# Kernel tuning notes

Hardware: AMD Instinct MI355X
Metric: run time of the kernel (lower is better)

Reference implementation:

```python
import jax, jax.numpy as jnp
import numpy as np

N = 50000      # nodes
E = 800000     # edges (before self-loops)
NFEATS = 256
NHIDS = 32
NHEADS = 8
NOUT = 128
NEG_SLOPE = 0.2


def leaky_relu(x, slope=NEG_SLOPE):
    return jnp.where(x >= 0, x, slope * x)


def gat_layer(x, src, dst, W, a_src, a_dst, b, heads, out_ch, concat):
    """PyG GATConv: h = xW; e_ij = LeakyReLU(a_s.h_j + a_d.h_i); softmax over
    edges grouped by destination; out_i = sum_j alpha_ij h_j (+bias)."""
    n = x.shape[0]
    h = (x @ W.T).reshape(n, heads, out_ch)            # [N,H,C]
    al_s = jnp.einsum('nhc,hc->nh', h, a_src)          # [N,H]
    al_d = jnp.einsum('nhc,hc->nh', h, a_dst)          # [N,H]
    e = leaky_relu(al_s[src] + al_d[dst])              # [E',H]
    e_max = jax.ops.segment_max(e, dst, num_segments=n)
    e_max = jnp.where(jnp.isfinite(e_max), e_max, 0.0)
    ex = jnp.exp(e - e_max[dst])
    denom = jax.ops.segment_sum(ex, dst, num_segments=n)
    alpha = ex / (denom[dst] + 1e-16)                  # [E',H]
    msg = h[src] * alpha[:, :, None]                   # [E',H,C]
    out = jax.ops.segment_sum(msg, dst, num_segments=n)  # [N,H,C]
    if concat:
        out = out.reshape(n, heads * out_ch)
    else:
        out = out.mean(axis=1)
    return out + b


def setup_inputs() -> dict:
    key = jax.random.key(0)
    ks = jax.random.split(key, 12)
    edge_index = jax.random.randint(ks[0], (2, E), 0, N, dtype=jnp.int64)
    x = jax.random.normal(ks[1], (N, NFEATS), dtype=jnp.float32)
    s1 = 1.0 / np.sqrt(NFEATS)
    W1 = jax.random.uniform(ks[2], (NHEADS * NHIDS, NFEATS), jnp.float32, -s1, s1)
    att_src1 = jax.random.normal(ks[3], (NHEADS, NHIDS), jnp.float32) * 0.1
    att_dst1 = jax.random.normal(ks[4], (NHEADS, NHIDS), jnp.float32) * 0.1
    b1 = jnp.zeros((NHEADS * NHIDS,), jnp.float32)
    s2 = 1.0 / np.sqrt(NHEADS * NHIDS)
    W2 = jax.random.uniform(ks[5], (NOUT, NHEADS * NHIDS), jnp.float32, -s2, s2)
    att_src2 = jax.random.normal(ks[6], (1, NOUT), jnp.float32) * 0.1
    att_dst2 = jax.random.normal(ks[7], (1, NOUT), jnp.float32) * 0.1
    b2 = jnp.zeros((NOUT,), jnp.float32)
    return {"edge_index": edge_index, "x": x,
            "W1": W1, "att_src1": att_src1, "att_dst1": att_dst1, "b1": b1,
            "W2": W2, "att_src2": att_src2, "att_dst2": att_dst2, "b2": b2}


def reference(edge_index, x, W1, att_src1, att_dst1, b1, W2, att_src2, att_dst2, b2):
    n = x.shape[0]
    loops = jnp.arange(n, dtype=edge_index.dtype)
    src = jnp.concatenate([edge_index[0], loops])  # PyG adds self-loops
    dst = jnp.concatenate([edge_index[1], loops])
    h = gat_layer(x, src, dst, W1, att_src1, att_dst1, b1, NHEADS, NHIDS, True)
    h = leaky_relu(h)  # module activation, slope 0.2
    # dropout(p=0.6, train=False) -> identity in eval mode
    out = gat_layer(h, src, dst, W2, att_src2, att_dst2, b2, 1, NOUT, True)
    return out
```

## Files before the change

kernel.cpp:

```cpp
#include <hip/hip_runtime.h>
#include <hip/hip_bf16.h>
#include <math.h>

#define NN 50000
#define EE 800000
#define ET 850000
#define NFEATS 256
#define NHIDS 32
#define NHEADS 8
#define NOUT 128

typedef __attribute__((ext_vector_type(8))) short bf16x8;
typedef __attribute__((ext_vector_type(4))) float f32x4;
typedef __attribute__((ext_vector_type(8))) unsigned short ushort8_t;

__device__ inline ushort f2bf(float x) {
    __hip_bfloat16 b = __float2bfloat16(x);
    return *reinterpret_cast<ushort*>(&b);
}
__device__ inline float bf2f(ushort u) {
    unsigned v = ((unsigned)u) << 16;
    return __builtin_bit_cast(float, v);
}
__device__ inline float bflo(unsigned u) {
    return __builtin_bit_cast(float, u << 16);
}
__device__ inline float bfhi(unsigned u) {
    return __builtin_bit_cast(float, u & 0xffff0000u);
}

#define NW1 (256 * 256)
#define NW2 (128 * 256)
__global__ void k_prep(const int* __restrict__ ei, int* __restrict__ deg,
                       const float* __restrict__ W1, ushort* __restrict__ W1h,
                       ushort* __restrict__ W1l,
                       const float* __restrict__ W2, ushort* __restrict__ W2h,
                       ushort* __restrict__ W2l) {
    int i = blockIdx.x * blockDim.x + threadIdx.x;
    if (i < ET) {
        int d = (i < EE) ? ei[EE + i] : (i - EE);
        atomicAdd(&deg[d], 1);
    } else if (i < ET + NW1) {
        int j = i - ET;
        float v = W1[j];
        ushort h = f2bf(v);
        W1h[j] = h;
        W1l[j] = f2bf(v - bf2f(h));
    } else if (i < ET + NW1 + NW2) {
        int j = i - ET - NW1;
        float v = W2[j];
        ushort h = f2bf(v);
        W2h[j] = h;
        W2l[j] = f2bf(v - bf2f(h));
    }
}

__global__ void k_scan_block(const int* __restrict__ deg, int* __restrict__ offsets,
                             int* __restrict__ bsum, int n) {
    __shared__ int lds[1024];
    int i = blockIdx.x * 1024 + threadIdx.x;
    int v = (i < n) ? deg[i] : 0;
    lds[threadIdx.x] = v;
    __syncthreads();
    for (int off = 1; off < 1024; off <<= 1) {
        int t = 0;
        if ((int)threadIdx.x >= off) t = lds[threadIdx.x - off];
        __syncthreads();
        lds[threadIdx.x] += t;
        __syncthreads();
    }
    if (i < n) offsets[i] = lds[threadIdx.x] - v;
    if (threadIdx.x == 1023) bsum[blockIdx.x] = lds[1023];
}

__global__ void k_scan_bsums(int* __restrict__ bsum, int nb) {
    int t = threadIdx.x;
    int v0 = (t < nb) ? bsum[t] : 0;
    int v = v0;
    for (int off = 1; off < 64; off <<= 1) {
        int u = __shfl_up(v, off, 64);
        if (t >= off) v += u;
    }
    if (t < nb) bsum[t] = v - v0;
}

__global__ void k_add_off(int* __restrict__ offsets, const int* __restrict__ bsum,
                          int n, int total) {
    int i = blockIdx.x * blockDim.x + threadIdx.x;
    if (i < n) offsets[i] += bsum[i >> 10];
    if (i == 0) offsets[n] = total;
}

__global__ void k_scatter(const int* __restrict__ ei, const int* __restrict__ offsets,
                          int* __restrict__ cursor, int* __restrict__ srcs) {
    int e = blockIdx.x * blockDim.x + threadIdx.x;
    if (e >= ET) return;
    int d, s;
    if (e < EE) { d = ei[EE + e]; s = ei[e]; }
    else        { d = e - EE;     s = e - EE; }
    int pos = offsets[d] + atomicAdd(&cursor[d], 1);
    srcs[pos] = s;
}

template <int TBN>
__global__ __launch_bounds__(512) void gemm_fused(const float* __restrict__ A,
                                                  const ushort* __restrict__ Wh,
                                                  const ushort* __restrict__ Wl,
                                                  ushort* __restrict__ Cb,
                                                  float* __restrict__ als,
                                                  float* __restrict__ ald,
                                                  const float* __restrict__ aS,
                                                  const float* __restrict__ aD,
                                                  int M) {
    constexpr int K = 256;
    constexpr int WN = TBN / 4;
    constexpr int NF = WN / 16;
    __shared__ ushort Ah[128][40], Al[128][40];
    __shared__ ushort Bh[TBN][40], Bl[TBN][40];
    __shared__ float att_red[256];

    int tid = threadIdx.x;
    int wid = tid >> 6, lane = tid & 63;
    int wm = wid >> 2, wn = wid & 3;
    int m0 = blockIdx.x * 128;

    f32x4 acc[4][NF];
#pragma unroll
    for (int i = 0; i < 4; i++)
#pragma unroll
        for (int j = 0; j < NF; j++) acc[i][j] = (f32x4){0.f, 0.f, 0.f, 0.f};

    for (int k0 = 0; k0 < K; k0 += 32) {
#pragma unroll
        for (int i = 0; i < 2; i++) {
            int s = tid + 512 * i;
            int r = s >> 3, c4 = s & 7;
            float4 v = make_float4(0.f, 0.f, 0.f, 0.f);
            if (m0 + r < M) v = *(const float4*)(A + (size_t)(m0 + r) * K + k0 + c4 * 4);
            ushort4 hi, lo;
            hi.x = f2bf(v.x); lo.x = f2bf(v.x - bf2f(hi.x));
            hi.y = f2bf(v.y); lo.y = f2bf(v.y - bf2f(hi.y));
            hi.z = f2bf(v.z); lo.z = f2bf(v.z - bf2f(hi.z));
            hi.w = f2bf(v.w); lo.w = f2bf(v.w - bf2f(hi.w));
            *(ushort4*)&Ah[r][c4 * 4] = hi;
            *(ushort4*)&Al[r][c4 * 4] = lo;
        }
        if constexpr (TBN == 256) {
            int r = tid >> 1, c16 = (tid & 1) * 16;
            const ushort* gh = Wh + (size_t)r * K + k0 + c16;
            const ushort* gl = Wl + (size_t)r * K + k0 + c16;
            *(ushort8_t*)&Bh[r][c16]     = *(const ushort8_t*)gh;
            *(ushort8_t*)&Bh[r][c16 + 8] = *(const ushort8_t*)(gh + 8);
            *(ushort8_t*)&Bl[r][c16]     = *(const ushort8_t*)gl;
            *(ushort8_t*)&Bl[r][c16 + 8] = *(const ushort8_t*)(gl + 8);
        } else {
            int s = tid & 255;
            int r = s >> 1, c16 = (s & 1) * 16;
            const ushort* gp = ((tid < 256) ? Wh : Wl) + (size_t)r * K + k0 + c16;
            ushort* lp = ((tid < 256) ? &Bh[r][c16] : &Bl[r][c16]);
            *(ushort8_t*)lp       = *(const ushort8_t*)gp;
            *(ushort8_t*)(lp + 8) = *(const ushort8_t*)(gp + 8);
        }
        __syncthreads();

        int koff = (lane >> 4) * 8;
        int rsel = lane & 15;
        bf16x8 ah[4], al[4], bh[NF], bl[NF];
#pragma unroll
        for (int mf = 0; mf < 4; mf++) {
            int r = wm * 64 + mf * 16 + rsel;
            ah[mf] = *(const bf16x8*)&Ah[r][koff];
            al[mf] = *(const bf16x8*)&Al[r][koff];
        }
#pragma unroll
        for (int nf = 0; nf < NF; nf++) {
            int c = wn * WN + nf * 16 + rsel;
            bh[nf] = *(const bf16x8*)&Bh[c][koff];
            bl[nf] = *(const bf16x8*)&Bl[c][koff];
        }
#pragma unroll
        for (int mf = 0; mf < 4; mf++)
#pragma unroll
            for (int nf = 0; nf < NF; nf++) {
                acc[mf][nf] = __builtin_amdgcn_mfma_f32_16x16x32_bf16(ah[mf], bh[nf], acc[mf][nf], 0, 0, 0);
                acc[mf][nf] = __builtin_amdgcn_mfma_f32_16x16x32_bf16(ah[mf], bl[nf], acc[mf][nf], 0, 0, 0);
                acc[mf][nf] = __builtin_amdgcn_mfma_f32_16x16x32_bf16(al[mf], bh[nf], acc[mf][nf], 0, 0, 0);
            }
        __syncthreads();
    }

    int l15 = lane & 15, lhi = lane >> 4;

#pragma unroll
    for (int mf = 0; mf < 4; mf++) {
        int gr0 = m0 + wm * 64 + mf * 16 + lhi * 4;
#pragma unroll
        for (int nf = 0; nf < NF; nf++) {
            int gc = wn * WN + nf * 16 + l15;
#pragma unroll
            for (int j = 0; j < 4; j++)
                if (gr0 + j < M) Cb[(size_t)(gr0 + j) * TBN + gc] = f2bf(acc[mf][nf][j]);
        }
    }

    if constexpr (TBN == 256) {
        float as0 = aS[wn * 64 + l15],      as0b = aS[wn * 64 + 16 + l15];
        float as1 = aS[wn * 64 + 32 + l15], as1b = aS[wn * 64 + 48 + l15];
        float ad0 = aD[wn * 64 + l15],      ad0b = aD[wn * 64 + 16 + l15];
        float ad1 = aD[wn * 64 + 32 + l15], ad1b = aD[wn * 64 + 48 + l15];
#pragma unroll
        for (int mf = 0; mf < 4; mf++) {
#pragma unroll
            for (int j = 0; j < 4; j++) {
                float ps0 = acc[mf][0][j] * as0 + acc[mf][1][j] * as0b;
                float ps1 = acc[mf][2][j] * as1 + acc[mf][3][j] * as1b;
                float pd0 = acc[mf][0][j] * ad0 + acc[mf][1][j] * ad0b;
                float pd1 = acc[mf][2][j] * ad1 + acc[mf][3][j] * ad1b;
#pragma unroll
                for (int off = 1; off <= 8; off <<= 1) {
                    ps0 += __shfl_xor(ps0, off, 64);
                    ps1 += __shfl_xor(ps1, off, 64);
                    pd0 += __shfl_xor(pd0, off, 64);
                    pd1 += __shfl_xor(pd1, off, 64);
                }
                int gr = m0 + wm * 64 + mf * 16 + lhi * 4 + j;
                if (l15 == 0 && gr < M) {
                    als[gr * 8 + 2 * wn]     = ps0;
                    als[gr * 8 + 2 * wn + 1] = ps1;
                    ald[gr * 8 + 2 * wn]     = pd0;
                    ald[gr * 8 + 2 * wn + 1] = pd1;
                }
            }
        }
    } else {
        float asv0 = aS[wn * 32 + l15], asv1 = aS[wn * 32 + 16 + l15];
        float adv0 = aD[wn * 32 + l15], adv1 = aD[wn * 32 + 16 + l15];
        if (tid < 256) att_red[tid] = 0.f;
        __syncthreads();
#pragma unroll
        for (int mf = 0; mf < 4; mf++) {
#pragma unroll
            for (int j = 0; j < 4; j++) {
                float ps = acc[mf][0][j] * asv0 + acc[mf][1][j] * asv1;
                float pd = acc[mf][0][j] * adv0 + acc[mf][1][j] * adv1;
#pragma unroll
                for (int off = 1; off <= 8; off <<= 1) {
                    ps += __shfl_xor(ps, off, 64);
                    pd += __shfl_xor(pd, off, 64);
                }
                if (l15 == 0) {
                    int rl = wm * 64 + mf * 16 + lhi * 4 + j;
                    atomicAdd(&att_red[rl], ps);
                    atomicAdd(&att_red[128 + rl], pd);
                }
            }
        }
        __syncthreads();
        if (tid < 128 && m0 + tid < M) {
            als[m0 + tid] = att_red[tid];
            ald[m0 + tid] = att_red[128 + tid];
        }
    }
}

__global__ __launch_bounds__(128) void k_agg1(
    const ushort* __restrict__ h1b, const float* __restrict__ als,
    const float* __restrict__ ald, const int* __restrict__ offsets,
    const int* __restrict__ srcs, const float* __restrict__ b1,
    float* __restrict__ out1) {
    int lane = threadIdx.x & 63;
    int wv = threadIdx.x >> 6;
    int n = blockIdx.x * 2 + wv;
    int g = lane >> 5;
    int c32 = lane & 31;
    int head = c32 >> 2;
    int base = offsets[n], deg = offsets[n + 1] - base;

    int eL8 = lane >> 3;
    int hS = lane & 7;
    float aldS = ald[n * 8 + hS];

    float acc[8] = {0.f, 0.f, 0.f, 0.f, 0.f, 0.f, 0.f, 0.f};
    float dsum = 0.f;
    for (int chunk = 0; chunk < deg; chunk += 16) {
        int len = deg - chunk; if (len > 16) len = 16;
        int i0 = chunk + eL8;     if (i0 >= deg) i0 = deg - 1;
        int i1 = chunk + 8 + eL8; if (i1 >= deg) i1 = deg - 1;
        int sE0 = srcs[base + i0];
        int sE1 = srcs[base + i1];
        float v0 = als[sE0 * 8 + hS] + aldS;
        float v1 = als[sE1 * 8 + hS] + aldS;
        v0 = (v0 >= 0.f) ? v0 : 0.2f * v0;
        v1 = (v1 >= 0.f) ? v1 : 0.2f * v1;
        float w0 = __expf(v0), w1 = __expf(v1);
#pragma unroll
        for (int i = 0; i < 8; i++) {
            int e = 2 * i + g;
            int slot = (e & 7) * 8;
            int si = __shfl((i < 4) ? sE0 : sE1, slot, 64);
            float wi = __shfl((i < 4) ? w0 : w1, slot + head, 64);
            if (e >= len) wi = 0.f;
            uint4 hv = *(const uint4*)(h1b + (size_t)si * 256 + 8 * c32);
            acc[0] += wi * bflo(hv.x); acc[1] += wi * bfhi(hv.x);
            acc[2] += wi * bflo(hv.y); acc[3] += wi * bfhi(hv.y);
            acc[4] += wi * bflo(hv.z); acc[5] += wi * bfhi(hv.z);
            acc[6] += wi * bflo(hv.w); acc[7] += wi * bfhi(hv.w);
            dsum += wi;
        }
    }
#pragma unroll
    for (int j = 0; j < 8; j++) acc[j] += __shfl_xor(acc[j], 32, 64);
    dsum += __shfl_xor(dsum, 32, 64);

    if (g == 0) {
        float inv = 1.f / (dsum + 1e-16f);
        const float* bb = b1 + 8 * c32;
        float r[8];
#pragma unroll
        for (int j = 0; j < 8; j++) {
            float t = acc[j] * inv + bb[j];
            r[j] = (t >= 0.f) ? t : 0.2f * t;
        }
        float* o = out1 + (size_t)n * 256 + 8 * c32;
        *(float4*)o       = make_float4(r[0], r[1], r[2], r[3]);
        *(float4*)(o + 4) = make_float4(r[4], r[5], r[6], r[7]);
    }
}

__global__ __launch_bounds__(128) void k_agg2(
    const ushort* __restrict__ h2b, const float* __restrict__ als,
    const float* __restrict__ ald, const int* __restrict__ offsets,
    const int* __restrict__ srcs, const float* __restrict__ b2,
    float* __restrict__ out) {
    int lane = threadIdx.x & 63;
    int wv = threadIdx.x >> 6;
    int n = blockIdx.x * 2 + wv;
    int g = lane >> 4;
    int c16 = lane & 15;
    int base = offsets[n], deg = offsets[n + 1] - base;
    float aldv = ald[n];

    float acc[8] = {0.f, 0.f, 0.f, 0.f, 0.f, 0.f, 0.f, 0.f};
    float dsum = 0.f;
    for (int chunk = 0; chunk < deg; chunk += 16) {
        int len = deg - chunk; if (len > 16) len = 16;
        int idx = chunk + c16; if (idx >= deg) idx = deg - 1;
        int sE = srcs[base + idx];
        float v = als[sE] + aldv;
        v = (v >= 0.f) ? v : 0.2f * v;
        float wE = __expf(v);
#pragma unroll
        for (int i = 0; i < 4; i++) {
            int e = 4 * i + g;
            int si = __shfl(sE, e, 64);
            float wi = __shfl(wE, e, 64);
            if (e >= len) wi = 0.f;
            uint4 hv = *(const uint4*)(h2b + (size_t)si * 128 + 8 * c16);
            acc[0] += wi * bflo(hv.x); acc[1] += wi * bfhi(hv.x);
            acc[2] += wi * bflo(hv.y); acc[3] += wi * bfhi(hv.y);
            acc[4] += wi * bflo(hv.z); acc[5] += wi * bfhi(hv.z);
            acc[6] += wi * bflo(hv.w); acc[7] += wi * bfhi(hv.w);
            dsum += wi;
        }
    }
#pragma unroll
    for (int j = 0; j < 8; j++) {
        acc[j] += __shfl_xor(acc[j], 16, 64);
        acc[j] += __shfl_xor(acc[j], 32, 64);
    }
    dsum += __shfl_xor(dsum, 16, 64);
    dsum += __shfl_xor(dsum, 32, 64);

    if (g == 0) {
        float inv = 1.f / (dsum + 1e-16f);
        const float* bb = b2 + 8 * c16;
        float r[8];
#pragma unroll
        for (int j = 0; j < 8; j++) r[j] = acc[j] * inv + bb[j];
        float* o = out + (size_t)n * 128 + 8 * c16;
        *(float4*)o       = make_float4(r[0], r[1], r[2], r[3]);
        *(float4*)(o + 4) = make_float4(r[4], r[5], r[6], r[7]);
    }
}

extern "C" void kernel_launch(void* const* d_in, const int* in_sizes, int n_in,
                              void* d_out, int out_size, void* d_ws, size_t ws_size,
                              hipStream_t stream) {
    const int* ei = (const int*)d_in[0];
    const float* x = (const float*)d_in[1];
    const float* W1 = (const float*)d_in[2];
    const float* aS1 = (const float*)d_in[3];
    const float* aD1 = (const float*)d_in[4];
    const float* b1 = (const float*)d_in[5];
    const float* W2 = (const float*)d_in[6];
    const float* aS2 = (const float*)d_in[7];
    const float* aD2 = (const float*)d_in[8];
    const float* b2 = (const float*)d_in[9];
    float* out = (float*)d_out;

    char* w = (char*)d_ws;
    auto alloc = [&](size_t bytes) {
        char* p = w;
        w += (bytes + 255) & ~(size_t)255;
        return p;
    };
    ushort* h1b  = (ushort*)alloc((size_t)NN * 256 * 2);
    float*  out1 = (float*)alloc((size_t)NN * 256 * 4);
    float*  als1 = (float*)alloc((size_t)NN * 8 * 4);
    float*  ald1 = (float*)alloc((size_t)NN * 8 * 4);
    int* deg     = (int*)alloc((size_t)(NN + 1) * 4);
    int* offsets = (int*)alloc((size_t)(NN + 1) * 4);
    int* cursor  = (int*)alloc((size_t)NN * 4);
    int* srcs    = (int*)alloc((size_t)ET * 4);
    int* bsum    = (int*)alloc(64 * 4);
    ushort* W1h  = (ushort*)alloc((size_t)NW1 * 2);
    ushort* W1l  = (ushort*)alloc((size_t)NW1 * 2);
    ushort* W2h  = (ushort*)alloc((size_t)NW2 * 2);
    ushort* W2l  = (ushort*)alloc((size_t)NW2 * 2);
    ushort* h2b = h1b;
    float* als2 = als1;
    float* ald2 = ald1;

    const int nb = (NN + 1023) / 1024;

    hipMemsetAsync(deg, 0, (size_t)NN * 4, stream);
    hipMemsetAsync(cursor, 0, (size_t)NN * 4, stream);

    const int prep_total = ET + NW1 + NW2;
    k_prep<<<(prep_total + 255) / 256, 256, 0, stream>>>(ei, deg, W1, W1h, W1l, W2, W2h, W2l);

    k_scan_block<<<nb, 1024, 0, stream>>>(deg, offsets, bsum, NN);
    k_scan_bsums<<<1, 64, 0, stream>>>(bsum, nb);
    k_add_off<<<(NN + 255) / 256, 256, 0, stream>>>(offsets, bsum, NN, ET);
    k_scatter<<<(ET + 255) / 256, 256, 0, stream>>>(ei, offsets, cursor, srcs);

    gemm_fused<256><<<(NN + 127) / 128, 512, 0, stream>>>(x, W1h, W1l, h1b, als1, ald1, aS1, aD1, NN);
    k_agg1<<<NN / 2, 128, 0, stream>>>(h1b, als1, ald1, offsets, srcs, b1, out1);

    gemm_fused<128><<<(NN + 127) / 128, 512, 0, stream>>>(out1, W2h, W2l, h2b, als2, ald2, aS2, aD2, NN);
    k_agg2<<<NN / 2, 128, 0, stream>>>(h2b, als2, ald2, offsets, srcs, b2, out);
}
```

Baseline: 271.8 us.

## Emit layer-1 output as bf16 hi/lo split and record edge ranks for scatter

The first aggregation kernel now writes its activated output directly as bf16 high/low pairs, so the second GEMM loads pre-split operands instead of reading fp32 and splitting per tile. Separately, the degree-counting atomic now saves each edge's rank, so the scatter kernel writes positions without a second atomic pass and the cursor memset is dropped. The costs are an extra 850k-int rank buffer written and read, and a different GEMM A-load path for the layer-2 instantiation. Total bytes for the intermediate stay the same (two bf16 arrays versus one fp32 array).

```diff
diff --git a/kernel.cpp b/kernel.cpp
--- a/kernel.cpp
+++ b/kernel.cpp
@@ -32,6 +32,7 @@
 #define NW1 (256 * 256)
 #define NW2 (128 * 256)
 __global__ void k_prep(const int* __restrict__ ei, int* __restrict__ deg,
+                       int* __restrict__ rank,
                        const float* __restrict__ W1, ushort* __restrict__ W1h,
                        ushort* __restrict__ W1l,
                        const float* __restrict__ W2, ushort* __restrict__ W2h,
@@ -39,7 +40,7 @@
     int i = blockIdx.x * blockDim.x + threadIdx.x;
     if (i < ET) {
         int d = (i < EE) ? ei[EE + i] : (i - EE);
-        atomicAdd(&deg[d], 1);
+        rank[i] = atomicAdd(&deg[d], 1);
     } else if (i < ET + NW1) {
         int j = i - ET;
         float v = W1[j];
@@ -92,18 +93,19 @@
 }
 
 __global__ void k_scatter(const int* __restrict__ ei, const int* __restrict__ offsets,
-                          int* __restrict__ cursor, int* __restrict__ srcs) {
+                          const int* __restrict__ rank, int* __restrict__ srcs) {
     int e = blockIdx.x * blockDim.x + threadIdx.x;
     if (e >= ET) return;
     int d, s;
     if (e < EE) { d = ei[EE + e]; s = ei[e]; }
     else        { d = e - EE;     s = e - EE; }
-    int pos = offsets[d] + atomicAdd(&cursor[d], 1);
-    srcs[pos] = s;
+    srcs[offsets[d] + rank[e]] = s;
 }
 
 template <int TBN>
-__global__ __launch_bounds__(512) void gemm_fused(const float* __restrict__ A,
+__global__ __launch_bounds__(512) void gemm_fused(const float* __restrict__ Af,
+                                                  const ushort* __restrict__ Agh,
+                                                  const ushort* __restrict__ Agl,
                                                   const ushort* __restrict__ Wh,
                                                   const ushort* __restrict__ Wl,
                                                   ushort* __restrict__ Cb,
@@ -131,19 +133,31 @@
         for (int j = 0; j < NF; j++) acc[i][j] = (f32x4){0.f, 0.f, 0.f, 0.f};
 
     for (int k0 = 0; k0 < K; k0 += 32) {
-#pragma unroll
-        for (int i = 0; i < 2; i++) {
-            int s = tid + 512 * i;
-            int r = s >> 3, c4 = s & 7;
-            float4 v = make_float4(0.f, 0.f, 0.f, 0.f);
-            if (m0 + r < M) v = *(const float4*)(A + (size_t)(m0 + r) * K + k0 + c4 * 4);
-            ushort4 hi, lo;
-            hi.x = f2bf(v.x); lo.x = f2bf(v.x - bf2f(hi.x));
-            hi.y = f2bf(v.y); lo.y = f2bf(v.y - bf2f(hi.y));
-            hi.z = f2bf(v.z); lo.z = f2bf(v.z - bf2f(hi.z));
-            hi.w = f2bf(v.w); lo.w = f2bf(v.w - bf2f(hi.w));
-            *(ushort4*)&Ah[r][c4 * 4] = hi;
-            *(ushort4*)&Al[r][c4 * 4] = lo;
+        if constexpr (TBN == 256) {
+#pragma unroll
+            for (int i = 0; i < 2; i++) {
+                int s = tid + 512 * i;
+                int r = s >> 3, c4 = s & 7;
+                float4 v = make_float4(0.f, 0.f, 0.f, 0.f);
+                if (m0 + r < M) v = *(const float4*)(Af + (size_t)(m0 + r) * K + k0 + c4 * 4);
+                ushort4 hi, lo;
+                hi.x = f2bf(v.x); lo.x = f2bf(v.x - bf2f(hi.x));
+                hi.y = f2bf(v.y); lo.y = f2bf(v.y - bf2f(hi.y));
+                hi.z = f2bf(v.z); lo.z = f2bf(v.z - bf2f(hi.z));
+                hi.w = f2bf(v.w); lo.w = f2bf(v.w - bf2f(hi.w));
+                *(ushort4*)&Ah[r][c4 * 4] = hi;
+                *(ushort4*)&Al[r][c4 * 4] = lo;
+            }
+        } else {
+            int r = tid >> 2, c8 = (tid & 3) * 8;
+            ushort8_t vh = {0, 0, 0, 0, 0, 0, 0, 0};
+            ushort8_t vl = {0, 0, 0, 0, 0, 0, 0, 0};
+            if (m0 + r < M) {
+                vh = *(const ushort8_t*)(Agh + (size_t)(m0 + r) * K + k0 + c8);
+                vl = *(const ushort8_t*)(Agl + (size_t)(m0 + r) * K + k0 + c8);
+            }
+            *(ushort8_t*)&Ah[r][c8] = vh;
+            *(ushort8_t*)&Al[r][c8] = vl;
         }
         if constexpr (TBN == 256) {
             int r = tid >> 1, c16 = (tid & 1) * 16;
@@ -267,7 +281,7 @@
     const ushort* __restrict__ h1b, const float* __restrict__ als,
     const float* __restrict__ ald, const int* __restrict__ offsets,
     const int* __restrict__ srcs, const float* __restrict__ b1,
-    float* __restrict__ out1) {
+    ushort* __restrict__ out1h, ushort* __restrict__ out1l) {
     int lane = threadIdx.x & 63;
     int wv = threadIdx.x >> 6;
     int n = blockIdx.x * 2 + wv;
@@ -315,15 +329,17 @@
     if (g == 0) {
         float inv = 1.f / (dsum + 1e-16f);
         const float* bb = b1 + 8 * c32;
-        float r[8];
+        ushort8_t vh, vl;
 #pragma unroll
         for (int j = 0; j < 8; j++) {
             float t = acc[j] * inv + bb[j];
-            r[j] = (t >= 0.f) ? t : 0.2f * t;
-        }
-        float* o = out1 + (size_t)n * 256 + 8 * c32;
-        *(float4*)o       = make_float4(r[0], r[1], r[2], r[3]);
-        *(float4*)(o + 4) = make_float4(r[4], r[5], r[6], r[7]);
+            float r = (t >= 0.f) ? t : 0.2f * t;
+            ushort h = f2bf(r);
+            vh[j] = h;
+            vl[j] = f2bf(r - bf2f(h));
+        }
+        *(ushort8_t*)(out1h + (size_t)n * 256 + 8 * c32) = vh;
+        *(ushort8_t*)(out1l + (size_t)n * 256 + 8 * c32) = vl;
     }
 }
 
@@ -404,13 +420,14 @@
         w += (bytes + 255) & ~(size_t)255;
         return p;
     };
-    ushort* h1b  = (ushort*)alloc((size_t)NN * 256 * 2);
-    float*  out1 = (float*)alloc((size_t)NN * 256 * 4);
-    float*  als1 = (float*)alloc((size_t)NN * 8 * 4);
-    float*  ald1 = (float*)alloc((size_t)NN * 8 * 4);
+    ushort* h1b   = (ushort*)alloc((size_t)NN * 256 * 2);
+    ushort* out1h = (ushort*)alloc((size_t)NN * 256 * 2);
+    ushort* out1l = (ushort*)alloc((size_t)NN * 256 * 2);
+    float*  als1  = (float*)alloc((size_t)NN * 8 * 4);
+    float*  ald1  = (float*)alloc((size_t)NN * 8 * 4);
     int* deg     = (int*)alloc((size_t)(NN + 1) * 4);
     int* offsets = (int*)alloc((size_t)(NN + 1) * 4);
-    int* cursor  = (int*)alloc((size_t)NN * 4);
+    int* rank    = (int*)alloc((size_t)ET * 4);
     int* srcs    = (int*)alloc((size_t)ET * 4);
     int* bsum    = (int*)alloc(64 * 4);
     ushort* W1h  = (ushort*)alloc((size_t)NW1 * 2);
@@ -424,19 +441,18 @@
     const int nb = (NN + 1023) / 1024;
 
     hipMemsetAsync(deg, 0, (size_t)NN * 4, stream);
-    hipMemsetAsync(cursor, 0, (size_t)NN * 4, stream);
 
     const int prep_total = ET + NW1 + NW2;
-    k_prep<<<(prep_total + 255) / 256, 256, 0, stream>>>(ei, deg, W1, W1h, W1l, W2, W2h, W2l);
+    k_prep<<<(prep_total + 255) / 256, 256, 0, stream>>>(ei, deg, rank, W1, W1h, W1l, W2, W2h, W2l);
 
     k_scan_block<<<nb, 1024, 0, stream>>>(deg, offsets, bsum, NN);
     k_scan_bsums<<<1, 64, 0, stream>>>(bsum, nb);
     k_add_off<<<(NN + 255) / 256, 256, 0, stream>>>(offsets, bsum, NN, ET);
-    k_scatter<<<(ET + 255) / 256, 256, 0, stream>>>(ei, offsets, cursor, srcs);
-
-    gemm_fused<256><<<(NN + 127) / 128, 512, 0, stream>>>(x, W1h, W1l, h1b, als1, ald1, aS1, aD1, NN);
-    k_agg1<<<NN / 2, 128, 0, stream>>>(h1b, als1, ald1, offsets, srcs, b1, out1);
-
-    gemm_fused<128><<<(NN + 127) / 128, 512, 0, stream>>>(out1, W2h, W2l, h2b, als2, ald2, aS2, aD2, NN);
+    k_scatter<<<(ET + 255) / 256, 256, 0, stream>>>(ei, offsets, rank, srcs);
+
+    gemm_fused<256><<<(NN + 127) / 128, 512, 0, stream>>>(x, nullptr, nullptr, W1h, W1l, h1b, als1, ald1, aS1, aD1, NN);
+    k_agg1<<<NN / 2, 128, 0, stream>>>(h1b, als1, ald1, offsets, srcs, b1, out1h, out1l);
+
+    gemm_fused<128><<<(NN + 127) / 128, 512, 0, stream>>>(nullptr, out1h, out1l, W2h, W2l, h2b, als2, ald2, aS2, aD2, NN);
     k_agg2<<<NN / 2, 128, 0, stream>>>(h2b, als2, ald2, offsets, srcs, b2, out);
 }
```

Result: faster. 240.0 us (-11.7%).
